# Kernel tuning notes

Hardware: AMD Instinct MI355X
Metric: run time of the kernel (lower is better)

## Reference

```python
import jax, jax.numpy as jnp
import numpy as np
from jax import lax

WINDOW = 9
LOSS_WEIGHT = 1.0
EPS = 1e-05
BALANCE = 0.2

_DN = ('NCHW', 'OIHW', 'NCHW')

def _local_sum(x, k=WINDOW):
    # Separable box-filter sum == conv2d with ones((1,1,k,k)), padding=k//2.
    pad = k // 2
    kh = jnp.ones((1, 1, k, 1), x.dtype)
    kw = jnp.ones((1, 1, 1, k), x.dtype)
    y = lax.conv_general_dilated(x, kh, (1, 1), [(pad, pad), (0, 0)], dimension_numbers=_DN)
    return lax.conv_general_dilated(y, kw, (1, 1), [(0, 0), (pad, pad)], dimension_numbers=_DN)

def _lncc_loss(pred, target, k=WINDOW, eps=EPS):
    n = k * k
    pred_mean = _local_sum(pred, k) / n
    target_mean = _local_sum(target, k) / n
    # NOTE: faithful to source: variance uses raw local sum of squares minus mean^2
    pred_var = jnp.clip(_local_sum(pred * pred, k) - pred_mean * pred_mean, 0.0, None)
    target_var = jnp.clip(_local_sum(target * target, k) - target_mean * target_mean, 0.0, None)
    cov = _local_sum(pred * target, k) - pred_mean * target_mean
    lncc = cov / (jnp.sqrt(pred_var + eps) * jnp.sqrt(target_var + eps))
    return 1.0 - jnp.mean(lncc)

def setup_inputs() -> dict:
    key = jax.random.key(0)
    k1, k2, k3 = jax.random.split(key, 3)
    B, H, W = 16, 512, 512
    pred = jax.random.normal(k1, (B, 1, H, W), dtype=jnp.float32)
    target = jax.random.normal(k2, (B, 1, H, W), dtype=jnp.float32)
    mask = jax.random.normal(k3, (B, 2, H, W), dtype=jnp.float32)
    return {"pred": pred, "target": target, "mask": mask}

def reference(pred, target, mask):
    m = jnp.argmax(mask, axis=1)[:, None].astype(pred.dtype)  # [B,1,H,W]
    p_pred1 = (1.0 - m) * pred
    p_pred2 = (1.0 - m) * target
    n_pred1 = m * pred
    n_pred2 = m * target
    return LOSS_WEIGHT * (BALANCE * _lncc_loss(p_pred1, p_pred2)
                          - (1.0 - BALANCE) * _lncc_loss(n_pred1, n_pred2))
```

## Files before the change

### kernel.cpp

```cpp
#include <hip/hip_runtime.h>

#define NB   16
#define NH   512
#define NW   512
#define RAD  4
#define BH   8
#define NBANDS (NH / BH)
#define NBLOCKS (NB * NBANDS)
#define EPSF 1e-5f

__device__ __forceinline__ float lncc_val(float Sa, float Sb, float Saa, float Sbb, float Sab) {
    const float inv_n = 1.0f / 81.0f;
    float ma  = Sa * inv_n;
    float mb  = Sb * inv_n;
    float va  = fmaxf(Saa - ma * ma, 0.0f);
    float vb  = fmaxf(Sbb - mb * mb, 0.0f);
    float cov = Sab - ma * mb;
    return cov * rsqrtf((va + EPSF) * (vb + EPSF));
}

template<int SGN>
__device__ __forceinline__ void accum_row(const float* __restrict__ prow,
                                          const float* __restrict__ trow,
                                          const float* __restrict__ mrow,
                                          size_t hw, int y, int col0,
                                          float (&V)[10][8])
{
    size_t off = (size_t)y * NW + col0;
    float4 p0 = *reinterpret_cast<const float4*>(prow + off);
    float4 p1 = *reinterpret_cast<const float4*>(prow + off + 4);
    float4 t0 = *reinterpret_cast<const float4*>(trow + off);
    float4 t1 = *reinterpret_cast<const float4*>(trow + off + 4);
    float4 a0 = *reinterpret_cast<const float4*>(mrow + off);
    float4 a1 = *reinterpret_cast<const float4*>(mrow + off + 4);
    float4 b0 = *reinterpret_cast<const float4*>(mrow + off + hw);
    float4 b1 = *reinterpret_cast<const float4*>(mrow + off + hw + 4);

    float p[8]  = {p0.x,p0.y,p0.z,p0.w, p1.x,p1.y,p1.z,p1.w};
    float t[8]  = {t0.x,t0.y,t0.z,t0.w, t1.x,t1.y,t1.z,t1.w};
    float c0[8] = {a0.x,a0.y,a0.z,a0.w, a1.x,a1.y,a1.z,a1.w};
    float c1[8] = {b0.x,b0.y,b0.z,b0.w, b1.x,b1.y,b1.z,b1.w};

    #pragma unroll
    for (int c = 0; c < 8; ++c) {
        float pv = p[c], tv = t[c];
        float s  = (c1[c] > c0[c]) ? 1.0f : 0.0f;
        float pp = pv * pv, tt = tv * tv, pt = pv * tv;
        if (SGN > 0) {
            V[0][c] += pv; V[1][c] += tv; V[2][c] += pp; V[3][c] += tt; V[4][c] += pt;
            V[5][c] = fmaf(s, pv, V[5][c]); V[6][c] = fmaf(s, tv, V[6][c]);
            V[7][c] = fmaf(s, pp, V[7][c]); V[8][c] = fmaf(s, tt, V[8][c]);
            V[9][c] = fmaf(s, pt, V[9][c]);
        } else {
            V[0][c] -= pv; V[1][c] -= tv; V[2][c] -= pp; V[3][c] -= tt; V[4][c] -= pt;
            V[5][c] = fmaf(-s, pv, V[5][c]); V[6][c] = fmaf(-s, tv, V[6][c]);
            V[7][c] = fmaf(-s, pp, V[7][c]); V[8][c] = fmaf(-s, tt, V[8][c]);
            V[9][c] = fmaf(-s, pt, V[9][c]);
        }
    }
}

__global__ __launch_bounds__(64)
void lncc_main(const float* __restrict__ pred,
               const float* __restrict__ targ,
               const float* __restrict__ mask,
               float* __restrict__ part)
{
    const int lane = threadIdx.x;
    const int col0 = lane * 8;
    const int b    = blockIdx.x / NBANDS;
    const int y0   = (blockIdx.x % NBANDS) * BH;

    const size_t hw   = (size_t)NH * NW;
    const float* prow = pred + (size_t)b * hw;
    const float* trow = targ + (size_t)b * hw;
    const float* mrow = mask + (size_t)b * 2 * hw;

    float V[10][8];
    #pragma unroll
    for (int q = 0; q < 10; ++q)
        #pragma unroll
        for (int c = 0; c < 8; ++c) V[q][c] = 0.0f;

    #pragma unroll
    for (int j = -RAD; j < RAD; ++j) {
        int y = y0 + j;
        if (y >= 0) accum_row<1>(prow, trow, mrow, hw, y, col0, V);
    }

    float sum_p = 0.0f, sum_n = 0.0f;

    for (int r = 0; r < BH; ++r) {
        int y  = y0 + r;
        int ye = y + RAD;
        if (ye < NH) accum_row<1>(prow, trow, mrow, hw, ye, col0, V);

        {
            float HhA[10][4];
            #pragma unroll
            for (int q = 0; q < 10; ++q) {
                float hp0 = __shfl_up(V[q][4], 1);
                float hp1 = __shfl_up(V[q][5], 1);
                float hp2 = __shfl_up(V[q][6], 1);
                float hp3 = __shfl_up(V[q][7], 1);
                hp0 = (lane > 0) ? hp0 : 0.0f;
                hp1 = (lane > 0) ? hp1 : 0.0f;
                hp2 = (lane > 0) ? hp2 : 0.0f;
                hp3 = (lane > 0) ? hp3 : 0.0f;
                float h = ((hp0 + hp1) + (hp2 + hp3))
                        + ((V[q][0] + V[q][1]) + (V[q][2] + V[q][3])) + V[q][4];
                HhA[q][0] = h;
                h += V[q][5] - hp0; HhA[q][1] = h;
                h += V[q][6] - hp1; HhA[q][2] = h;
                h += V[q][7] - hp2; HhA[q][3] = h;
            }
            #pragma unroll
            for (int c = 0; c < 4; ++c) {
                float Sa=HhA[0][c], Sb=HhA[1][c], Saa=HhA[2][c], Sbb=HhA[3][c], Sab=HhA[4][c];
                float Ma=HhA[5][c], Mb=HhA[6][c], Maa=HhA[7][c], Mbb=HhA[8][c], Mab=HhA[9][c];
                sum_n += lncc_val(Ma, Mb, Maa, Mbb, Mab);
                sum_p += lncc_val(Sa-Ma, Sb-Mb, Saa-Maa, Sbb-Mbb, Sab-Mab);
            }
        }

        {
            float HhB[10][4];
            #pragma unroll
            for (int q = 0; q < 10; ++q) {
                float hn0 = __shfl_down(V[q][0], 1);
                float hn1 = __shfl_down(V[q][1], 1);
                float hn2 = __shfl_down(V[q][2], 1);
                float hn3 = __shfl_down(V[q][3], 1);
                hn0 = (lane < 63) ? hn0 : 0.0f;
                hn1 = (lane < 63) ? hn1 : 0.0f;
                hn2 = (lane < 63) ? hn2 : 0.0f;
                hn3 = (lane < 63) ? hn3 : 0.0f;
                float h = ((V[q][0] + V[q][1]) + (V[q][2] + V[q][3]))
                        + ((V[q][4] + V[q][5]) + (V[q][6] + V[q][7])) + hn0;
                HhB[q][0] = h;
                h += hn1 - V[q][0]; HhB[q][1] = h;
                h += hn2 - V[q][1]; HhB[q][2] = h;
                h += hn3 - V[q][2]; HhB[q][3] = h;
            }
            #pragma unroll
            for (int c = 0; c < 4; ++c) {
                float Sa=HhB[0][c], Sb=HhB[1][c], Saa=HhB[2][c], Sbb=HhB[3][c], Sab=HhB[4][c];
                float Ma=HhB[5][c], Mb=HhB[6][c], Maa=HhB[7][c], Mbb=HhB[8][c], Mab=HhB[9][c];
                sum_n += lncc_val(Ma, Mb, Maa, Mbb, Mab);
                sum_p += lncc_val(Sa-Ma, Sb-Mb, Saa-Maa, Sbb-Mbb, Sab-Mab);
            }
        }

        if (r < BH - 1) {
            int yl = y - RAD;
            if (yl >= 0) accum_row<-1>(prow, trow, mrow, hw, yl, col0, V);
        }
    }

    #pragma unroll
    for (int off = 32; off > 0; off >>= 1) {
        sum_p += __shfl_down(sum_p, off, 64);
        sum_n += __shfl_down(sum_n, off, 64);
    }
    if (lane == 0) {
        part[blockIdx.x]           = sum_p;
        part[NBLOCKS + blockIdx.x] = sum_n;
    }
}

__global__ void lncc_finalize(const float* __restrict__ part, float* __restrict__ out) {
    __shared__ float w[8];
    int tid = threadIdx.x;
    float sp = 0.0f, sn = 0.0f;
    for (int i = tid; i < NBLOCKS; i += 256) {
        sp += part[i];
        sn += part[NBLOCKS + i];
    }
    #pragma unroll
    for (int off = 32; off > 0; off >>= 1) {
        sp += __shfl_down(sp, off, 64);
        sn += __shfl_down(sn, off, 64);
    }
    int wave = tid >> 6, lane = tid & 63;
    if (lane == 0) { w[wave] = sp; w[4 + wave] = sn; }
    __syncthreads();
    if (tid == 0) {
        double SP = (double)w[0] + (double)w[1] + (double)w[2] + (double)w[3];
        double SN = (double)w[4] + (double)w[5] + (double)w[6] + (double)w[7];
        const double npix = (double)NB * (double)NH * (double)NW;
        double mp = SP / npix;
        double mn = SN / npix;
        out[0] = (float)(0.2 * (1.0 - mp) - 0.8 * (1.0 - mn));
    }
}

extern "C" void kernel_launch(void* const* d_in, const int* in_sizes, int n_in,
                              void* d_out, int out_size, void* d_ws, size_t ws_size,
                              hipStream_t stream) {
    const float* pred = (const float*)d_in[0];
    const float* targ = (const float*)d_in[1];
    const float* mask = (const float*)d_in[2];
    float* part = (float*)d_ws;

    lncc_main<<<dim3(NBLOCKS), dim3(64), 0, stream>>>(pred, targ, mask, part);
    lncc_finalize<<<dim3(1), dim3(256), 0, stream>>>(part, (float*)d_out);
}
```

Before: 117.6 us.

## Prefetch next rows with clamped branchless loads and halve band height

Row loads are split from accumulation. The next entering row and the current leaving row are now loaded before the compute of the current step so memory latency overlaps with arithmetic. Out-of-range rows are clamped to a valid address and zeroed by a validity weight, which removes the branches. The band height drops from 8 to 4 rows to double the block count, and launch bounds request 2 waves per EU. This raises halo overhead (4 rows computed per 12 rows loaded) and register pressure from holding two prefetched rows.

```diff
diff --git a/kernel.cpp b/kernel.cpp
--- a/kernel.cpp
+++ b/kernel.cpp
@@ -4,7 +4,7 @@
 #define NH   512
 #define NW   512
 #define RAD  4
-#define BH   8
+#define BH   4
 #define NBANDS (NH / BH)
 #define NBLOCKS (NB * NBANDS)
 #define EPSF 1e-5f
@@ -19,14 +19,16 @@
     return cov * rsqrtf((va + EPSF) * (vb + EPSF));
 }
 
-template<int SGN>
-__device__ __forceinline__ void accum_row(const float* __restrict__ prow,
-                                          const float* __restrict__ trow,
-                                          const float* __restrict__ mrow,
-                                          size_t hw, int y, int col0,
-                                          float (&V)[10][8])
+struct RowData { float p[8]; float t[8]; float s[8]; };
+
+__device__ __forceinline__ RowData load_row(const float* __restrict__ prow,
+                                            const float* __restrict__ trow,
+                                            const float* __restrict__ mrow,
+                                            size_t hw, int y, int col0)
 {
-    size_t off = (size_t)y * NW + col0;
+    RowData R;
+    int yc = y < 0 ? 0 : (y > NH - 1 ? NH - 1 : y);
+    size_t off = (size_t)yc * NW + col0;
     float4 p0 = *reinterpret_cast<const float4*>(prow + off);
     float4 p1 = *reinterpret_cast<const float4*>(prow + off + 4);
     float4 t0 = *reinterpret_cast<const float4*>(trow + off);
@@ -36,31 +38,39 @@
     float4 b0 = *reinterpret_cast<const float4*>(mrow + off + hw);
     float4 b1 = *reinterpret_cast<const float4*>(mrow + off + hw + 4);
 
+    float vw = (y >= 0 && y < NH) ? 1.0f : 0.0f;
     float p[8]  = {p0.x,p0.y,p0.z,p0.w, p1.x,p1.y,p1.z,p1.w};
     float t[8]  = {t0.x,t0.y,t0.z,t0.w, t1.x,t1.y,t1.z,t1.w};
     float c0[8] = {a0.x,a0.y,a0.z,a0.w, a1.x,a1.y,a1.z,a1.w};
     float c1[8] = {b0.x,b0.y,b0.z,b0.w, b1.x,b1.y,b1.z,b1.w};
-
     #pragma unroll
     for (int c = 0; c < 8; ++c) {
-        float pv = p[c], tv = t[c];
-        float s  = (c1[c] > c0[c]) ? 1.0f : 0.0f;
+        R.p[c] = p[c] * vw;
+        R.t[c] = t[c] * vw;
+        R.s[c] = (c1[c] > c0[c]) ? 1.0f : 0.0f;
+    }
+    return R;
+}
+
+template<int SGN>
+__device__ __forceinline__ void accum(const RowData& R, float (&V)[10][8]) {
+    #pragma unroll
+    for (int c = 0; c < 8; ++c) {
+        float pv = R.p[c], tv = R.t[c];
+        float s  = (SGN > 0) ? R.s[c] : -R.s[c];
         float pp = pv * pv, tt = tv * tv, pt = pv * tv;
         if (SGN > 0) {
             V[0][c] += pv; V[1][c] += tv; V[2][c] += pp; V[3][c] += tt; V[4][c] += pt;
-            V[5][c] = fmaf(s, pv, V[5][c]); V[6][c] = fmaf(s, tv, V[6][c]);
-            V[7][c] = fmaf(s, pp, V[7][c]); V[8][c] = fmaf(s, tt, V[8][c]);
-            V[9][c] = fmaf(s, pt, V[9][c]);
         } else {
             V[0][c] -= pv; V[1][c] -= tv; V[2][c] -= pp; V[3][c] -= tt; V[4][c] -= pt;
-            V[5][c] = fmaf(-s, pv, V[5][c]); V[6][c] = fmaf(-s, tv, V[6][c]);
-            V[7][c] = fmaf(-s, pp, V[7][c]); V[8][c] = fmaf(-s, tt, V[8][c]);
-            V[9][c] = fmaf(-s, pt, V[9][c]);
-        }
-    }
-}
-
-__global__ __launch_bounds__(64)
+        }
+        V[5][c] = fmaf(s, pv, V[5][c]); V[6][c] = fmaf(s, tv, V[6][c]);
+        V[7][c] = fmaf(s, pp, V[7][c]); V[8][c] = fmaf(s, tt, V[8][c]);
+        V[9][c] = fmaf(s, pt, V[9][c]);
+    }
+}
+
+__global__ __launch_bounds__(64, 2)
 void lncc_main(const float* __restrict__ pred,
                const float* __restrict__ targ,
                const float* __restrict__ mask,
@@ -84,19 +94,25 @@
 
     #pragma unroll
     for (int j = -RAD; j < RAD; ++j) {
-        int y = y0 + j;
-        if (y >= 0) accum_row<1>(prow, trow, mrow, hw, y, col0, V);
+        RowData w = load_row(prow, trow, mrow, hw, y0 + j, col0);
+        accum<1>(w, V);
     }
 
     float sum_p = 0.0f, sum_n = 0.0f;
-
+    RowData e = load_row(prow, trow, mrow, hw, y0 + RAD, col0);
+
+    #pragma unroll
     for (int r = 0; r < BH; ++r) {
-        int y  = y0 + r;
-        int ye = y + RAD;
-        if (ye < NH) accum_row<1>(prow, trow, mrow, hw, ye, col0, V);
+        RowData l, en;
+        if (r < BH - 1) {
+            l  = load_row(prow, trow, mrow, hw, y0 + r - RAD, col0);
+            en = load_row(prow, trow, mrow, hw, y0 + r + RAD + 1, col0);
+        }
+
+        accum<1>(e, V);
 
         {
-            float HhA[10][4];
+            float Hh[10][4];
             #pragma unroll
             for (int q = 0; q < 10; ++q) {
                 float hp0 = __shfl_up(V[q][4], 1);
@@ -109,22 +125,22 @@
                 hp3 = (lane > 0) ? hp3 : 0.0f;
                 float h = ((hp0 + hp1) + (hp2 + hp3))
                         + ((V[q][0] + V[q][1]) + (V[q][2] + V[q][3])) + V[q][4];
-                HhA[q][0] = h;
-                h += V[q][5] - hp0; HhA[q][1] = h;
-                h += V[q][6] - hp1; HhA[q][2] = h;
-                h += V[q][7] - hp2; HhA[q][3] = h;
+                Hh[q][0] = h;
+                h += V[q][5] - hp0; Hh[q][1] = h;
+                h += V[q][6] - hp1; Hh[q][2] = h;
+                h += V[q][7] - hp2; Hh[q][3] = h;
             }
             #pragma unroll
             for (int c = 0; c < 4; ++c) {
-                float Sa=HhA[0][c], Sb=HhA[1][c], Saa=HhA[2][c], Sbb=HhA[3][c], Sab=HhA[4][c];
-                float Ma=HhA[5][c], Mb=HhA[6][c], Maa=HhA[7][c], Mbb=HhA[8][c], Mab=HhA[9][c];
+                float Sa=Hh[0][c], Sb=Hh[1][c], Saa=Hh[2][c], Sbb=Hh[3][c], Sab=Hh[4][c];
+                float Ma=Hh[5][c], Mb=Hh[6][c], Maa=Hh[7][c], Mbb=Hh[8][c], Mab=Hh[9][c];
                 sum_n += lncc_val(Ma, Mb, Maa, Mbb, Mab);
                 sum_p += lncc_val(Sa-Ma, Sb-Mb, Saa-Maa, Sbb-Mbb, Sab-Mab);
             }
         }
 
         {
-            float HhB[10][4];
+            float Hh[10][4];
             #pragma unroll
             for (int q = 0; q < 10; ++q) {
                 float hn0 = __shfl_down(V[q][0], 1);
@@ -137,23 +153,23 @@
                 hn3 = (lane < 63) ? hn3 : 0.0f;
                 float h = ((V[q][0] + V[q][1]) + (V[q][2] + V[q][3]))
                         + ((V[q][4] + V[q][5]) + (V[q][6] + V[q][7])) + hn0;
-                HhB[q][0] = h;
-                h += hn1 - V[q][0]; HhB[q][1] = h;
-                h += hn2 - V[q][1]; HhB[q][2] = h;
-                h += hn3 - V[q][2]; HhB[q][3] = h;
+                Hh[q][0] = h;
+                h += hn1 - V[q][0]; Hh[q][1] = h;
+                h += hn2 - V[q][1]; Hh[q][2] = h;
+                h += hn3 - V[q][2]; Hh[q][3] = h;
             }
             #pragma unroll
             for (int c = 0; c < 4; ++c) {
-                float Sa=HhB[0][c], Sb=HhB[1][c], Saa=HhB[2][c], Sbb=HhB[3][c], Sab=HhB[4][c];
-                float Ma=HhB[5][c], Mb=HhB[6][c], Maa=HhB[7][c], Mbb=HhB[8][c], Mab=HhB[9][c];
+                float Sa=Hh[0][c], Sb=Hh[1][c], Saa=Hh[2][c], Sbb=Hh[3][c], Sab=Hh[4][c];
+                float Ma=Hh[5][c], Mb=Hh[6][c], Maa=Hh[7][c], Mbb=Hh[8][c], Mab=Hh[9][c];
                 sum_n += lncc_val(Ma, Mb, Maa, Mbb, Mab);
                 sum_p += lncc_val(Sa-Ma, Sb-Mb, Saa-Maa, Sbb-Mbb, Sab-Mab);
             }
         }
 
         if (r < BH - 1) {
-            int yl = y - RAD;
-            if (yl >= 0) accum_row<-1>(prow, trow, mrow, hw, yl, col0, V);
+            accum<-1>(l, V);
+            e = en;
         }
     }
 
```

New measurement: 284.8 us. 142% more time.
